# Performance work log

Measured on AMD Instinct MI355X. Metric: run time of the kernel, lower is better.

Reference implementation:

```python
import math
import jax, jax.numpy as jnp
import numpy as np
from jax import lax

B, L = 8192, 512          # batch, seq_len; configs.d_model == seq_len (forced by LayerNorm over last dim)
TREND_POLY = 3
F_LEN = L // 2 - 1        # rfft bins after slicing [low_freq=1 : -1] for even t
TOP_K = int(math.log(F_LEN))  # = 5


def setup_inputs() -> dict:
    key = jax.random.key(0)
    ks = jax.random.split(key, 12)
    s = 0.02
    return {
        "x": jax.random.normal(ks[0], (B, L, 1), dtype=jnp.float32),
        "conv1_w": jax.random.normal(ks[1], (TREND_POLY, 1, 3), dtype=jnp.float32) * s,
        "conv1_b": jnp.zeros((TREND_POLY,), dtype=jnp.float32),
        "conv3_w": jax.random.normal(ks[2], (L, L, 3), dtype=jnp.float32) * s,
        "conv3_b": jnp.zeros((L,), dtype=jnp.float32),
        "w1": jax.random.normal(ks[3], (L, L), dtype=jnp.float32) * s,
        "b1": jnp.zeros((L,), dtype=jnp.float32),
        "w2": jax.random.normal(ks[4], (L, L), dtype=jnp.float32) * s,
        "b2": jnp.zeros((L,), dtype=jnp.float32),
        "ln_g": jnp.ones((L,), dtype=jnp.float32),
        "ln_b": jnp.zeros((L,), dtype=jnp.float32),
    }


def _gelu(x):
    return jax.nn.gelu(x, approximate=False)  # torch nn.GELU default (erf)


def _conv1d(x, w, b):
    # x: (b, Cin, T), w: (Cout, Cin, 3), padding=1
    y = lax.conv_general_dilated(x, w, window_strides=(1,), padding=[(1, 1)],
                                 dimension_numbers=("NCH", "OIH", "NCH"))
    return y + b[None, :, None]


def _trend_block(xp, conv1_w, conv1_b, conv3_w, conv3_b):
    # xp: (b, 1, L)
    h = _gelu(_conv1d(xp, conv1_w, conv1_b))        # (b, 3, L)
    h = h.transpose(0, 2, 1)                         # (b, L, 3) -- channels = seq_len
    h = _conv1d(h, conv3_w, conv3_b)                 # (b, L, 3)
    # poly_space: lin_space = [1/(out_dim+1)] = [0.5]; powers 1..3 -> (3, 1)
    lin = jnp.array([0.5], dtype=xp.dtype)
    poly = jnp.stack([lin ** (p + 1) for p in range(TREND_POLY)], axis=0)  # (3,1)
    # torch: (b,L,3) @ (3,1) -> (b,L,1) -> transpose -> (b,1,L)
    return jnp.einsum("blp,po->bol", h, poly)        # (b, 1, L)


def _fourier_layer(x):
    # x: (b, t, d=1); low_freq=1, t even
    b, t, d = x.shape
    xf = jnp.fft.rfft(x, axis=1)[:, 1:-1]            # (b, F, d) complex
    freqs = jnp.fft.rfftfreq(t).astype(x.dtype)[1:-1]  # (F,)
    mag = jnp.abs(xf)                                # (b, F, d)
    _, idx = lax.top_k(mag.transpose(0, 2, 1), TOP_K)  # (b, d, k)
    idx = idx.transpose(0, 2, 1)                     # (b, k, d)
    xf_sel = jnp.take_along_axis(xf, idx, axis=1)    # (b, k, d)
    f_sel = freqs[idx]                               # (b, k, d)
    # extrapolate with conjugate-symmetric pairs
    xf2 = jnp.concatenate([xf_sel, jnp.conj(xf_sel)], axis=1)       # (b, 2k, d)
    f2 = jnp.concatenate([f_sel, -f_sel], axis=1)[:, :, None, :]    # (b, 2k, 1, d)
    tt = jnp.arange(t, dtype=x.dtype)[None, None, :, None]          # (1, 1, t, 1)
    amp = jnp.abs(xf2)[:, :, None, :]                               # (b, 2k, 1, d)
    phase = jnp.arctan2(xf2.imag, xf2.real)[:, :, None, :]
    x_time = amp * jnp.cos(2.0 * math.pi * f2 * tt + phase)         # (b, 2k, t, d)
    return jnp.sum(x_time, axis=1)                                  # (b, t, d)


def reference(x, conv1_w, conv1_b, conv3_w, conv3_b, w1, b1, w2, b2, ln_g, ln_b):
    xp = x.transpose(0, 2, 1)                        # (b, 1, L)
    trend = _trend_block(xp, conv1_w, conv1_b, conv3_w, conv3_b)    # (b, 1, L)
    season = _fourier_layer(x).transpose(0, 2, 1)    # (b, 1, L)
    # residual MLP branch on enc_out = (b, 1, L); LayerNorm over last dim (== d_model)
    e = xp
    mu = jnp.mean(e, axis=-1, keepdims=True)
    var = jnp.mean((e - mu) ** 2, axis=-1, keepdims=True)
    ln = (e - mu) * lax.rsqrt(var + 1e-5) * ln_g + ln_b
    m = _gelu(jnp.einsum("bcl,ol->bco", ln, w1) + b1)
    m = jnp.einsum("bcl,ol->bco", m, w2) + b2        # dropout is identity at eval
    e = e + m
    mean = jnp.mean(e, axis=1, keepdims=True)        # dim 1 has size 1 -> mean == e
    return (e - mean, season, trend, mean)
```

## Files before the change

### kernel.cpp

```cpp
#include <hip/hip_runtime.h>
#include <hip/hip_bf16.h>
#include <math.h>

#define B_ 8192
#define L_ 512
#define BL_ (B_ * L_)
#define KT_ 1536

using bf16x8 = __attribute__((ext_vector_type(8))) short;
using f32x4  = __attribute__((ext_vector_type(4))) float;

__device__ __forceinline__ float gelu_f(float v) {
    return 0.5f * v * (1.0f + erff(v * 0.70710678118654752f));
}
__device__ __forceinline__ float bf2f(unsigned short u) {
    return __uint_as_float(((unsigned int)u) << 16);
}
__device__ __forceinline__ unsigned short f2bf(float f) {
    unsigned int x = __float_as_uint(f);
    x += 0x7fffu + ((x >> 16) & 1u);
    return (unsigned short)(x >> 16);
}
__device__ __forceinline__ void gload16(const void* g, void* l) {
    __builtin_amdgcn_global_load_lds(
        (const __attribute__((address_space(1))) unsigned int*)g,
        (__attribute__((address_space(3))) unsigned int*)l, 16, 0, 0);
}

__global__ __launch_bounds__(256) void k_pre(const float* __restrict__ x,
        const float* __restrict__ c1w, const float* __restrict__ c1b,
        const float* __restrict__ lg, const float* __restrict__ lbias,
        unsigned short* __restrict__ h1, unsigned short* __restrict__ lnx) {
    __shared__ float xs[512];
    __shared__ float red[8];
    const int tid = threadIdx.x;
    const long b = blockIdx.x;
    const float* xr = x + (b << 9);
    float x0 = xr[tid], x1 = xr[tid + 256];
    xs[tid] = x0; xs[tid + 256] = x1;
    float s = x0 + x1, ss = x0 * x0 + x1 * x1;
#pragma unroll
    for (int off = 32; off > 0; off >>= 1) {
        s += __shfl_xor(s, off);
        ss += __shfl_xor(ss, off);
    }
    if ((tid & 63) == 0) { red[tid >> 6] = s; red[4 + (tid >> 6)] = ss; }
    __syncthreads();
    s  = red[0] + red[1] + red[2] + red[3];
    ss = red[4] + red[5] + red[6] + red[7];
    const float mu = s * (1.f / 512.f);
    const float rs = rsqrtf(ss * (1.f / 512.f) - mu * mu + 1e-5f);
    float w[9], cb[3];
#pragma unroll
    for (int j = 0; j < 9; ++j) w[j] = c1w[j];
#pragma unroll
    for (int j = 0; j < 3; ++j) cb[j] = c1b[j];
#pragma unroll
    for (int half = 0; half < 2; ++half) {
        const int i = tid + (half << 8);
        const float xm = i ? xs[i - 1] : 0.f;
        const float xc = xs[i];
        const float xp = (i != 511) ? xs[i + 1] : 0.f;
        unsigned short* hb = h1 + b * KT_ + i;
#pragma unroll
        for (int c = 0; c < 3; ++c) {
            float v = w[c * 3] * xm + w[c * 3 + 1] * xc + w[c * 3 + 2] * xp + cb[c];
            hb[(long)c << 9] = f2bf(gelu_f(v));
        }
        lnx[(b << 9) + i] = f2bf(fmaf((xc - mu) * rs, lg[i], lbias[i]));
    }
}

__global__ __launch_bounds__(256) void k_prep(const float* __restrict__ c3w,
        const float* __restrict__ w1, const float* __restrict__ w2,
        unsigned short* __restrict__ weff, unsigned short* __restrict__ w1b,
        unsigned short* __restrict__ w2b,
        double2* __restrict__ tabd, float2* __restrict__ tab,
        float2* __restrict__ tab32) {
    int idx = blockIdx.x * 256 + threadIdx.x;
    if (idx < 512) {
        double sv, cv;
        sincos((double)idx * (3.14159265358979323846 / 256.0), &sv, &cv);
        tabd[idx] = make_double2(cv, sv);
        tab[idx] = make_float2((float)cv, (float)sv);
        if ((idx & 15) == 0) tab32[idx >> 4] = make_float2((float)cv, (float)sv);
    }
    int o = idx >> 9, i = idx & 511;
    const float* t = c3w + (size_t)idx * 3;
    float t0 = t[0], t1 = t[1], t2 = t[2];
    size_t base = (size_t)o * KT_ + i;
    weff[base]        = f2bf(0.25f * t0 + 0.5f * t1);
    weff[base + 512]  = f2bf(0.125f * t0 + 0.25f * t1 + 0.5f * t2);
    weff[base + 1024] = f2bf(0.125f * t1 + 0.25f * t2);
    w1b[idx] = f2bf(w1[idx]);
    w2b[idx] = f2bf(w2[idx]);
}

template<int EMODE, int KD>
__global__ __launch_bounds__(256) void k_mgemm(
        const unsigned short* __restrict__ A, const unsigned short* __restrict__ W,
        const float* __restrict__ bias, float sbias,
        const float* __restrict__ xres, void* __restrict__ Cp) {
    __shared__ short As[128][32];
    __shared__ short Bs[64][32];
    const int tid = threadIdx.x;
    const int lane = tid & 63;
    const int wid = tid >> 6;
    const int m0 = blockIdx.x << 7;
    const int n0 = blockIdx.y << 6;
    const int wm = (wid & 1) << 6;
    const int wn = (wid >> 1) << 5;
    f32x4 acc[4][2] = {};

    const int ra0 = tid >> 2,           ca0 = ((tid & 3) ^ ((ra0 ^ (ra0 >> 2)) & 3)) << 3;
    const int ra1 = (256 + tid) >> 2,   ca1 = ((tid & 3) ^ ((ra1 ^ (ra1 >> 2)) & 3)) << 3;
    const int rb  = tid >> 2,           cb  = ca0;
    const unsigned short* Ab = A + (size_t)m0 * KD;
    const unsigned short* Wb = W + (size_t)n0 * KD;
    const int fx = (lane & 3) ^ ((lane & 15) >> 2);
    const int kslot = (((lane >> 4) ^ fx) << 3);
    const int frow = lane & 15;

    for (int k0 = 0; k0 < KD; k0 += 32) {
        __syncthreads();
        gload16(Ab + (size_t)ra0 * KD + k0 + ca0, &As[ra0][(tid & 3) << 3]);
        gload16(Ab + (size_t)ra1 * KD + k0 + ca1, &As[ra1][(tid & 3) << 3]);
        gload16(Wb + (size_t)rb  * KD + k0 + cb,  &Bs[rb][(tid & 3) << 3]);
        __syncthreads();
        bf16x8 af[4], bfr[2];
#pragma unroll
        for (int m = 0; m < 4; ++m)
            af[m] = *(const bf16x8*)&As[wm + (m << 4) + frow][kslot];
#pragma unroll
        for (int n = 0; n < 2; ++n)
            bfr[n] = *(const bf16x8*)&Bs[wn + (n << 4) + frow][kslot];
#pragma unroll
        for (int m = 0; m < 4; ++m)
#pragma unroll
            for (int n = 0; n < 2; ++n)
                acc[m][n] = __builtin_amdgcn_mfma_f32_16x16x32_bf16(af[m], bfr[n], acc[m][n], 0, 0, 0);
    }

    const int col0 = n0 + wn + (lane & 15);
    const int rbase = m0 + wm + ((lane >> 4) << 2);
#pragma unroll
    for (int n = 0; n < 2; ++n) {
        const int col = col0 + (n << 4);
        const float bz = sbias * bias[col];
#pragma unroll
        for (int m = 0; m < 4; ++m) {
#pragma unroll
            for (int r = 0; r < 4; ++r) {
                const size_t row = rbase + (m << 4) + r;
                float v = acc[m][n][r] + bz;
                if (EMODE == 0) {
                    ((float*)Cp)[row * 512 + col] = v;
                } else if (EMODE == 1) {
                    ((unsigned short*)Cp)[row * 512 + col] = f2bf(gelu_f(v));
                } else {
                    ((float*)Cp)[row * 512 + col] = v + xres[row * 512 + col];
                }
            }
        }
    }
}

__global__ __launch_bounds__(256) void k_season(const float* __restrict__ x,
        const double2* __restrict__ gtabd, const float2* __restrict__ gtab,
        const float2* __restrict__ gtab32,
        float* __restrict__ out1, float* __restrict__ out0) {
    __shared__ float2 xp[2][256];
    __shared__ float2 tab[512];
    __shared__ float2 Ys[2][512];
    __shared__ unsigned long long wkey[2][4][5];
    __shared__ float2 wval[2][4][5];

    const int tid = threadIdx.x;
    const int w = tid >> 6, l = tid & 63;
    const long b = (long)blockIdx.x << 1;
    const float* xr0 = x + (b << 9);
    const float* xr1 = xr0 + 512;

    {
        const int t1s = tid >> 3, t0s = tid & 7;
        const int g = (t1s << 4) + t0s;
        xp[0][tid] = make_float2(xr0[g], xr0[g + 8]);
        xp[1][tid] = make_float2(xr1[g], xr1[g + 8]);
        tab[tid] = gtab[tid];
        tab[tid + 256] = gtab[tid + 256];
    }
    __syncthreads();

    const int rr = (w << 3) + (l & 7);
    const int t0 = l >> 3;
    float ra0 = 0.f, ia0 = 0.f, rb0 = 0.f, ib0 = 0.f;
    float ra1 = 0.f, ia1 = 0.f, rb1 = 0.f, ib1 = 0.f;
    int e32 = 0;
#pragma unroll
    for (int t1 = 0; t1 < 32; ++t1) {
        float2 wt = gtab32[e32];
        e32 = (e32 + rr) & 31;
        float2 v0 = xp[0][(t1 << 3) + t0];
        float2 v1 = xp[1][(t1 << 3) + t0];
        ra0 = fmaf(v0.x, wt.x, ra0); ia0 = fmaf(v0.x, wt.y, ia0);
        rb0 = fmaf(v0.y, wt.x, rb0); ib0 = fmaf(v0.y, wt.y, ib0);
        ra1 = fmaf(v1.x, wt.x, ra1); ia1 = fmaf(v1.x, wt.y, ia1);
        rb1 = fmaf(v1.y, wt.x, rb1); ib1 = fmaf(v1.y, wt.y, ib1);
    }
    Ys[0][(t0 << 5) + rr] = make_float2(ra0, -ia0);
    Ys[0][((t0 + 8) << 5) + rr] = make_float2(rb0, -ib0);
    Ys[1][(t0 << 5) + rr] = make_float2(ra1, -ia1);
    Ys[1][((t0 + 8) << 5) + rr] = make_float2(rb1, -ib1);

    const int k = ((l >> 3) << 5) + rr;
    double xre0 = 0.0, xim0 = 0.0, xre1 = 0.0, xim1 = 0.0;
    int e = 0;
#pragma unroll
    for (int t0i = 0; t0i < 16; ++t0i) {
        float2 y0 = Ys[0][(t0i << 5) + rr];
        float2 y1 = Ys[1][(t0i << 5) + rr];
        double2 wt = gtabd[e];
        e = (e + k) & 511;
        xre0 += (double)y0.x * wt.x + (double)y0.y * wt.y;
        xim0 += (double)y0.y * wt.x - (double)y0.x * wt.y;
        xre1 += (double)y1.x * wt.x + (double)y1.y * wt.y;
        xim1 += (double)y1.y * wt.x - (double)y1.x * wt.y;
    }

    unsigned long long key0 = 0, key1 = 0;
    if (k != 0) {
        double m0 = xre0 * xre0 + xim0 * xim0;
        double m1 = xre1 * xre1 + xim1 * xim1;
        key0 = (__double_as_longlong(m0) & ~0xFFFull) | (unsigned long long)(4095 - k);
        key1 = (__double_as_longlong(m1) & ~0xFFFull) | (unsigned long long)(4095 - k);
    }
    const float fre0 = (float)xre0, fim0 = (float)xim0;
    const float fre1 = (float)xre1, fim1 = (float)xim1;

    for (int rnd = 0; rnd < 5; ++rnd) {
        unsigned long long rk0 = key0, rk1 = key1;
#pragma unroll
        for (int off = 32; off > 0; off >>= 1) {
            unsigned long long o0 = __shfl_xor(rk0, off);
            unsigned long long o1 = __shfl_xor(rk1, off);
            rk0 = (o0 > rk0) ? o0 : rk0;
            rk1 = (o1 > rk1) ? o1 : rk1;
        }
        if (key0 == rk0 && rk0 != 0ull) {
            wkey[0][w][rnd] = rk0; wval[0][w][rnd] = make_float2(fre0, fim0); key0 = 0;
        }
        if (key1 == rk1 && rk1 != 0ull) {
            wkey[1][w][rnd] = rk1; wval[1][w][rnd] = make_float2(fre1, fim1); key1 = 0;
        }
    }
    __syncthreads();

#pragma unroll
    for (int row = 0; row < 2; ++row) {
        float4 sel[5];
        int h0 = 0, h1 = 0, h2 = 0, h3 = 0;
#pragma unroll
        for (int rnd = 0; rnd < 5; ++rnd) {
            unsigned long long c0 = wkey[row][0][h0], c1 = wkey[row][1][h1];
            unsigned long long c2 = wkey[row][2][h2], c3 = wkey[row][3][h3];
            unsigned long long bk = c0; int bw = 0;
            if (c1 > bk) { bk = c1; bw = 1; }
            if (c2 > bk) { bk = c2; bw = 2; }
            if (c3 > bk) { bk = c3; bw = 3; }
            const int hs = (bw == 0) ? h0 : (bw == 1) ? h1 : (bw == 2) ? h2 : h3;
            float2 v = wval[row][bw][hs];
            h0 += (bw == 0); h1 += (bw == 1); h2 += (bw == 2); h3 += (bw == 3);
            const int kk = 4095 - (int)(bk & 0xFFFull);
            sel[rnd] = make_float4((float)kk, v.x, v.y, 0.f);
        }
        const long ro = ((b + row) << 9);
#pragma unroll
        for (int half = 0; half < 2; ++half) {
            int t = tid + (half << 8);
            float acc = 0.f;
#pragma unroll
            for (int j = 0; j < 5; ++j) {
                float4 sj = sel[j];
                int kj = (int)sj.x;
                float2 wt = tab[(kj * t) & 511];
                acc += sj.y * wt.x - sj.z * wt.y;
            }
            out1[ro + t] = 2.f * acc;
            out0[ro + t] = 0.f;
        }
    }
}

extern "C" void kernel_launch(void* const* d_in, const int* in_sizes, int n_in,
                              void* d_out, int out_size, void* d_ws, size_t ws_size,
                              hipStream_t stream) {
    const float* x   = (const float*)d_in[0];
    const float* c1w = (const float*)d_in[1];
    const float* c1b = (const float*)d_in[2];
    const float* c3w = (const float*)d_in[3];
    const float* c3b = (const float*)d_in[4];
    const float* w1  = (const float*)d_in[5];
    const float* b1  = (const float*)d_in[6];
    const float* w2  = (const float*)d_in[7];
    const float* b2  = (const float*)d_in[8];
    const float* lg  = (const float*)d_in[9];
    const float* lb  = (const float*)d_in[10];

    float* out  = (float*)d_out;
    float* out1 = out + (long)BL_;
    float* out2 = out + 2L * BL_;
    float* out3 = out + 3L * BL_;

    double2* tabd = (double2*)d_ws;
    float2* tab   = (float2*)((char*)d_ws + 8192);
    float2* tab32 = (float2*)((char*)d_ws + 12288);

    unsigned short* h1   = (unsigned short*)d_out;
    unsigned short* weff = h1 + (size_t)B_ * KT_;
    unsigned short* w1b  = weff + (size_t)L_ * KT_;
    unsigned short* w2b  = w1b + (size_t)L_ * L_;
    unsigned short* lnx  = (unsigned short*)(out3);
    unsigned short* m1   = (unsigned short*)d_out;

    k_pre<<<B_, 256, 0, stream>>>(x, c1w, c1b, lg, lb, h1, lnx);
    k_prep<<<L_ * L_ / 256, 256, 0, stream>>>(c3w, w1, w2, weff, w1b, w2b,
                                              tabd, tab, tab32);
    k_mgemm<0, KT_><<<dim3(64, 8), 256, 0, stream>>>(h1, weff, c3b, 0.875f, nullptr, out2);
    k_mgemm<1, 512><<<dim3(64, 8), 256, 0, stream>>>(lnx, w1b, b1, 1.0f, nullptr, m1);
    k_mgemm<2, 512><<<dim3(64, 8), 256, 0, stream>>>(m1, w2b, b2, 1.0f, x, out3);
    k_season<<<B_ / 2, 256, 0, stream>>>(x, tabd, tab, tab32, out1, out);
}
```

Measured before the change: 126.0 us.

## Double GEMM K-tile depth and process four rows per season block

The MFMA GEMM now stages 64-wide K tiles with a new 8-chunk XOR swizzle and runs two MFMA sub-steps per tile, halving the number of barrier pairs per K loop. The season kernel handles four batch rows per block instead of two, packing pairs of rows into float4 LDS entries so each twiddle load and table lookup is shared across more rows. This trades higher register and LDS use, and therefore possibly lower occupancy, for less synchronisation and more reuse of the twiddle tables.

```diff
diff --git a/kernel.cpp b/kernel.cpp
--- a/kernel.cpp
+++ b/kernel.cpp
@@ -101,8 +101,8 @@
         const unsigned short* __restrict__ A, const unsigned short* __restrict__ W,
         const float* __restrict__ bias, float sbias,
         const float* __restrict__ xres, void* __restrict__ Cp) {
-    __shared__ short As[128][32];
-    __shared__ short Bs[64][32];
+    __shared__ short As[128][64];
+    __shared__ short Bs[64][64];
     const int tid = threadIdx.x;
     const int lane = tid & 63;
     const int wid = tid >> 6;
@@ -112,33 +112,45 @@
     const int wn = (wid >> 1) << 5;
     f32x4 acc[4][2] = {};
 
-    const int ra0 = tid >> 2,           ca0 = ((tid & 3) ^ ((ra0 ^ (ra0 >> 2)) & 3)) << 3;
-    const int ra1 = (256 + tid) >> 2,   ca1 = ((tid & 3) ^ ((ra1 ^ (ra1 >> 2)) & 3)) << 3;
-    const int rb  = tid >> 2,           cb  = ca0;
+    const int srow = tid >> 3;
+    const int schunk = tid & 7;
     const unsigned short* Ab = A + (size_t)m0 * KD;
     const unsigned short* Wb = W + (size_t)n0 * KD;
-    const int fx = (lane & 3) ^ ((lane & 15) >> 2);
-    const int kslot = (((lane >> 4) ^ fx) << 3);
     const int frow = lane & 15;
-
-    for (int k0 = 0; k0 < KD; k0 += 32) {
+    const int fsw = frow & 7;
+    const int s0 = lane >> 4;
+
+    for (int k0 = 0; k0 < KD; k0 += 64) {
         __syncthreads();
-        gload16(Ab + (size_t)ra0 * KD + k0 + ca0, &As[ra0][(tid & 3) << 3]);
-        gload16(Ab + (size_t)ra1 * KD + k0 + ca1, &As[ra1][(tid & 3) << 3]);
-        gload16(Wb + (size_t)rb  * KD + k0 + cb,  &Bs[rb][(tid & 3) << 3]);
+#pragma unroll
+        for (int seg = 0; seg < 4; ++seg) {
+            const int r = (seg << 5) + srow;
+            const int c = (schunk ^ (r & 7)) << 3;
+            gload16(Ab + (size_t)r * KD + k0 + c, &As[r][schunk << 3]);
+        }
+#pragma unroll
+        for (int seg = 0; seg < 2; ++seg) {
+            const int r = (seg << 5) + srow;
+            const int c = (schunk ^ (r & 7)) << 3;
+            gload16(Wb + (size_t)r * KD + k0 + c, &Bs[r][schunk << 3]);
+        }
         __syncthreads();
-        bf16x8 af[4], bfr[2];
-#pragma unroll
-        for (int m = 0; m < 4; ++m)
-            af[m] = *(const bf16x8*)&As[wm + (m << 4) + frow][kslot];
-#pragma unroll
-        for (int n = 0; n < 2; ++n)
-            bfr[n] = *(const bf16x8*)&Bs[wn + (n << 4) + frow][kslot];
-#pragma unroll
-        for (int m = 0; m < 4; ++m)
+#pragma unroll
+        for (int kk = 0; kk < 2; ++kk) {
+            bf16x8 af[4], bfr[2];
+            const int sl = (kk << 2) + s0;
+#pragma unroll
+            for (int m = 0; m < 4; ++m)
+                af[m] = *(const bf16x8*)&As[wm + (m << 4) + frow][(sl ^ fsw) << 3];
 #pragma unroll
             for (int n = 0; n < 2; ++n)
-                acc[m][n] = __builtin_amdgcn_mfma_f32_16x16x32_bf16(af[m], bfr[n], acc[m][n], 0, 0, 0);
+                bfr[n] = *(const bf16x8*)&Bs[wn + (n << 4) + frow][(sl ^ fsw) << 3];
+#pragma unroll
+            for (int m = 0; m < 4; ++m)
+#pragma unroll
+                for (int n = 0; n < 2; ++n)
+                    acc[m][n] = __builtin_amdgcn_mfma_f32_16x16x32_bf16(af[m], bfr[n], acc[m][n], 0, 0, 0);
+        }
     }
 
     const int col0 = n0 + wn + (lane & 15);
@@ -169,23 +181,26 @@
         const double2* __restrict__ gtabd, const float2* __restrict__ gtab,
         const float2* __restrict__ gtab32,
         float* __restrict__ out1, float* __restrict__ out0) {
-    __shared__ float2 xp[2][256];
+    __shared__ float4 xpA[256];
+    __shared__ float4 xpB[256];
     __shared__ float2 tab[512];
-    __shared__ float2 Ys[2][512];
-    __shared__ unsigned long long wkey[2][4][5];
-    __shared__ float2 wval[2][4][5];
+    __shared__ float4 YsA[512];
+    __shared__ float4 YsB[512];
+    __shared__ unsigned long long wkey[4][4][5];
+    __shared__ float2 wval[4][4][5];
 
     const int tid = threadIdx.x;
     const int w = tid >> 6, l = tid & 63;
-    const long b = (long)blockIdx.x << 1;
+    const long b = (long)blockIdx.x << 2;
     const float* xr0 = x + (b << 9);
     const float* xr1 = xr0 + 512;
+    const float* xr2 = xr0 + 1024;
+    const float* xr3 = xr0 + 1536;
 
     {
-        const int t1s = tid >> 3, t0s = tid & 7;
-        const int g = (t1s << 4) + t0s;
-        xp[0][tid] = make_float2(xr0[g], xr0[g + 8]);
-        xp[1][tid] = make_float2(xr1[g], xr1[g + 8]);
+        const int g = ((tid >> 3) << 4) + (tid & 7);
+        xpA[tid] = make_float4(xr0[g], xr0[g + 8], xr1[g], xr1[g + 8]);
+        xpB[tid] = make_float4(xr2[g], xr2[g + 8], xr3[g], xr3[g + 8]);
         tab[tid] = gtab[tid];
         tab[tid + 256] = gtab[tid + 256];
     }
@@ -193,70 +208,82 @@
 
     const int rr = (w << 3) + (l & 7);
     const int t0 = l >> 3;
-    float ra0 = 0.f, ia0 = 0.f, rb0 = 0.f, ib0 = 0.f;
-    float ra1 = 0.f, ia1 = 0.f, rb1 = 0.f, ib1 = 0.f;
+    float ar[4] = {}, ai[4] = {}, br[4] = {}, bi[4] = {};
     int e32 = 0;
 #pragma unroll
     for (int t1 = 0; t1 < 32; ++t1) {
         float2 wt = gtab32[e32];
         e32 = (e32 + rr) & 31;
-        float2 v0 = xp[0][(t1 << 3) + t0];
-        float2 v1 = xp[1][(t1 << 3) + t0];
-        ra0 = fmaf(v0.x, wt.x, ra0); ia0 = fmaf(v0.x, wt.y, ia0);
-        rb0 = fmaf(v0.y, wt.x, rb0); ib0 = fmaf(v0.y, wt.y, ib0);
-        ra1 = fmaf(v1.x, wt.x, ra1); ia1 = fmaf(v1.x, wt.y, ia1);
-        rb1 = fmaf(v1.y, wt.x, rb1); ib1 = fmaf(v1.y, wt.y, ib1);
-    }
-    Ys[0][(t0 << 5) + rr] = make_float2(ra0, -ia0);
-    Ys[0][((t0 + 8) << 5) + rr] = make_float2(rb0, -ib0);
-    Ys[1][(t0 << 5) + rr] = make_float2(ra1, -ia1);
-    Ys[1][((t0 + 8) << 5) + rr] = make_float2(rb1, -ib1);
+        float4 vA = xpA[(t1 << 3) + t0];
+        float4 vB = xpB[(t1 << 3) + t0];
+        ar[0] = fmaf(vA.x, wt.x, ar[0]); ai[0] = fmaf(vA.x, wt.y, ai[0]);
+        br[0] = fmaf(vA.y, wt.x, br[0]); bi[0] = fmaf(vA.y, wt.y, bi[0]);
+        ar[1] = fmaf(vA.z, wt.x, ar[1]); ai[1] = fmaf(vA.z, wt.y, ai[1]);
+        br[1] = fmaf(vA.w, wt.x, br[1]); bi[1] = fmaf(vA.w, wt.y, bi[1]);
+        ar[2] = fmaf(vB.x, wt.x, ar[2]); ai[2] = fmaf(vB.x, wt.y, ai[2]);
+        br[2] = fmaf(vB.y, wt.x, br[2]); bi[2] = fmaf(vB.y, wt.y, bi[2]);
+        ar[3] = fmaf(vB.z, wt.x, ar[3]); ai[3] = fmaf(vB.z, wt.y, ai[3]);
+        br[3] = fmaf(vB.w, wt.x, br[3]); bi[3] = fmaf(vB.w, wt.y, bi[3]);
+    }
+    YsA[(t0 << 5) + rr] = make_float4(ar[0], -ai[0], ar[1], -ai[1]);
+    YsA[((t0 + 8) << 5) + rr] = make_float4(br[0], -bi[0], br[1], -bi[1]);
+    YsB[(t0 << 5) + rr] = make_float4(ar[2], -ai[2], ar[3], -ai[3]);
+    YsB[((t0 + 8) << 5) + rr] = make_float4(br[2], -bi[2], br[3], -bi[3]);
 
     const int k = ((l >> 3) << 5) + rr;
-    double xre0 = 0.0, xim0 = 0.0, xre1 = 0.0, xim1 = 0.0;
+    double xre[4] = {}, xim[4] = {};
     int e = 0;
 #pragma unroll
     for (int t0i = 0; t0i < 16; ++t0i) {
-        float2 y0 = Ys[0][(t0i << 5) + rr];
-        float2 y1 = Ys[1][(t0i << 5) + rr];
+        float4 yA = YsA[(t0i << 5) + rr];
+        float4 yB = YsB[(t0i << 5) + rr];
         double2 wt = gtabd[e];
         e = (e + k) & 511;
-        xre0 += (double)y0.x * wt.x + (double)y0.y * wt.y;
-        xim0 += (double)y0.y * wt.x - (double)y0.x * wt.y;
-        xre1 += (double)y1.x * wt.x + (double)y1.y * wt.y;
-        xim1 += (double)y1.y * wt.x - (double)y1.x * wt.y;
-    }
-
-    unsigned long long key0 = 0, key1 = 0;
-    if (k != 0) {
-        double m0 = xre0 * xre0 + xim0 * xim0;
-        double m1 = xre1 * xre1 + xim1 * xim1;
-        key0 = (__double_as_longlong(m0) & ~0xFFFull) | (unsigned long long)(4095 - k);
-        key1 = (__double_as_longlong(m1) & ~0xFFFull) | (unsigned long long)(4095 - k);
-    }
-    const float fre0 = (float)xre0, fim0 = (float)xim0;
-    const float fre1 = (float)xre1, fim1 = (float)xim1;
+        xre[0] += (double)yA.x * wt.x + (double)yA.y * wt.y;
+        xim[0] += (double)yA.y * wt.x - (double)yA.x * wt.y;
+        xre[1] += (double)yA.z * wt.x + (double)yA.w * wt.y;
+        xim[1] += (double)yA.w * wt.x - (double)yA.z * wt.y;
+        xre[2] += (double)yB.x * wt.x + (double)yB.y * wt.y;
+        xim[2] += (double)yB.y * wt.x - (double)yB.x * wt.y;
+        xre[3] += (double)yB.z * wt.x + (double)yB.w * wt.y;
+        xim[3] += (double)yB.w * wt.x - (double)yB.z * wt.y;
+    }
+
+    unsigned long long key[4] = {};
+    float fre[4], fim[4];
+#pragma unroll
+    for (int r = 0; r < 4; ++r) {
+        if (k != 0) {
+            double m = xre[r] * xre[r] + xim[r] * xim[r];
+            key[r] = (__double_as_longlong(m) & ~0xFFFull)
+                   | (unsigned long long)(4095 - k);
+        }
+        fre[r] = (float)xre[r]; fim[r] = (float)xim[r];
+    }
 
     for (int rnd = 0; rnd < 5; ++rnd) {
-        unsigned long long rk0 = key0, rk1 = key1;
+        unsigned long long rk[4] = {key[0], key[1], key[2], key[3]};
 #pragma unroll
         for (int off = 32; off > 0; off >>= 1) {
-            unsigned long long o0 = __shfl_xor(rk0, off);
-            unsigned long long o1 = __shfl_xor(rk1, off);
-            rk0 = (o0 > rk0) ? o0 : rk0;
-            rk1 = (o1 > rk1) ? o1 : rk1;
-        }
-        if (key0 == rk0 && rk0 != 0ull) {
-            wkey[0][w][rnd] = rk0; wval[0][w][rnd] = make_float2(fre0, fim0); key0 = 0;
-        }
-        if (key1 == rk1 && rk1 != 0ull) {
-            wkey[1][w][rnd] = rk1; wval[1][w][rnd] = make_float2(fre1, fim1); key1 = 0;
+#pragma unroll
+            for (int r = 0; r < 4; ++r) {
+                unsigned long long o = __shfl_xor(rk[r], off);
+                rk[r] = (o > rk[r]) ? o : rk[r];
+            }
+        }
+#pragma unroll
+        for (int r = 0; r < 4; ++r) {
+            if (key[r] == rk[r] && rk[r] != 0ull) {
+                wkey[r][w][rnd] = rk[r];
+                wval[r][w][rnd] = make_float2(fre[r], fim[r]);
+                key[r] = 0;
+            }
         }
     }
     __syncthreads();
 
 #pragma unroll
-    for (int row = 0; row < 2; ++row) {
+    for (int row = 0; row < 4; ++row) {
         float4 sel[5];
         int h0 = 0, h1 = 0, h2 = 0, h3 = 0;
 #pragma unroll
@@ -328,5 +355,5 @@
     k_mgemm<0, KT_><<<dim3(64, 8), 256, 0, stream>>>(h1, weff, c3b, 0.875f, nullptr, out2);
     k_mgemm<1, 512><<<dim3(64, 8), 256, 0, stream>>>(lnx, w1b, b1, 1.0f, nullptr, m1);
     k_mgemm<2, 512><<<dim3(64, 8), 256, 0, stream>>>(m1, w2b, b2, 1.0f, x, out3);
-    k_season<<<B_ / 2, 256, 0, stream>>>(x, tabd, tab, tab32, out1, out);
-}
+    k_season<<<B_ / 4, 256, 0, stream>>>(x, tabd, tab, tab32, out1, out);
+}
```

Result: no change. 125.0 us (-0.8%).
